# Optimization experiments

Measured on AMD Instinct MI355X. Metric: run time of the kernel, lower is better.

## Reference

```python
import jax, jax.numpy as jnp
import numpy as np

N_G, K = 1024, 64
n_G, k = 32, 8          # n_G = sqrt(N_G), k = sqrt(K)
m = n_G * k             # 256
M = N_G * K             # 65536

def _mask_indices(k):
    # concentric square rings of a k x k grid; ring 0 = outermost
    ii, jj = np.meshgrid(np.arange(k), np.arange(k), indexing='ij')
    d = np.minimum(np.minimum(ii, jj), np.minimum(k - 1 - ii, k - 1 - jj))
    rings = [(d == r) for r in range((k + 1) // 2)]
    groups = np.array_split(np.arange(len(rings)), 3)  # outer / inter / inner ring groups
    merged = [np.any(np.stack([rings[i] for i in g]), axis=0) for g in groups]
    outer, inter, inner = merged
    flat = lambda msk: np.nonzero(msk.ravel())[0]
    return flat(inner), flat(inter), flat(outer)

IDX_INNER, IDX_INTER, IDX_OUTER = _mask_indices(k)  # sizes 4, 12, 48

def setup_inputs() -> dict:
    key = jax.random.key(0)
    ks = jax.random.split(key, 13)
    p = lambda kk, sh: 0.05 * jax.random.normal(kk, sh, dtype=jnp.float32)
    return {
        'pgi': jax.random.normal(ks[0], (32, M, 3), dtype=jnp.float32),
        'W_lift': p(ks[1], (3, 32)),   'b_lift': p(ks[2], (32,)),
        'W_code': p(ks[3], (96, 128)), 'b_code': p(ks[4], (128,)),
        'W_h1': p(ks[5], (128, 64)),   'b_h1': p(ks[6], (64,)),
        'W_h2': p(ks[7], (64, 32)),    'b_h2': p(ks[8], (32,)),
        'W_h3': p(ks[9], (32, 16)),    'b_h3': p(ks[10], (16,)),
        'W_h4': p(ks[11], (16, 3)),    'b_h4': jnp.zeros((3,), jnp.float32),
    }

def _lift_max(pts, W, b):
    # pts: [B, N_G, n_sel, 3] -> SMLP(3->32, leakyrelu 0.2) -> max over points
    h = jax.nn.leaky_relu(jnp.einsum('bgpc,cd->bgpd', pts, W) + b, 0.2)
    return h.max(axis=2)  # [B, N_G, 32]

def reference(pgi, W_lift, b_lift, W_code, b_code, W_h1, b_h1, W_h2, b_h2, W_h3, b_h3, W_h4, b_h4):
    B = pgi.shape[0]
    # pgi [B, M, 3] is a row-major m x m grid; partition into N_G blocks of k x k points
    grid = pgi.reshape(B, n_G, k, n_G, k, 3)
    blocks = grid.transpose(0, 1, 3, 2, 4, 5).reshape(B, N_G, K, 3)
    v_inner = _lift_max(blocks[:, :, IDX_INNER], W_lift, b_lift)
    v_inter = _lift_max(blocks[:, :, IDX_INTER], W_lift, b_lift)
    v_outer = _lift_max(blocks[:, :, IDX_OUTER], W_lift, b_lift)
    v = jnp.concatenate([v_inner, v_inter, v_outer], axis=-1)   # [B, N_G, 96]
    v_code = jax.nn.leaky_relu(v @ W_code + b_code, 0.2)        # [B, N_G, 128]
    h = jax.nn.relu(v_code @ W_h1 + b_h1)
    h = jax.nn.relu(h @ W_h2 + b_h2)
    h = jax.nn.relu(h @ W_h3 + b_h3)
    return h @ W_h4 + b_h4                                      # guidance_pts [B, N_G, 3]
```

## Files before the change

### kernel.cpp

```cpp
#include <hip/hip_runtime.h>
#include <math.h>

constexpr int SV  = 100;
constexpr int SC  = 132;
constexpr int SH1 = 68;
constexpr int SH2 = 36;
constexpr int SH3 = 20;

__global__ __launch_bounds__(256, 2)
void flatnet_fused(const float* __restrict__ pgi,
                   const float* __restrict__ Wl, const float* __restrict__ bl,
                   const float* __restrict__ Wc, const float* __restrict__ bc,
                   const float* __restrict__ W1, const float* __restrict__ b1,
                   const float* __restrict__ W2, const float* __restrict__ b2,
                   const float* __restrict__ W3, const float* __restrict__ b3,
                   const float* __restrict__ W4, const float* __restrict__ b4,
                   float* __restrict__ out)
{
    __shared__ float sA[64 * SV];
    __shared__ float sB[64 * SC];

    const int t   = threadIdx.x;
    const int blk = blockIdx.x;

    {
        const int ln = t >> 2;
        const int q  = t & 3;
        const int gn = blk * 64 + ln;
        const int b  = gn >> 10;
        const int g  = gn & 1023;
        const int gi = g >> 5, gj = g & 31;

        float w0[8], w1[8], w2[8], bb[8];
        #pragma unroll
        for (int d = 0; d < 8; ++d) {
            const int dd = q * 8 + d;
            w0[d] = Wl[dd];
            w1[d] = Wl[32 + dd];
            w2[d] = Wl[64 + dd];
            bb[d] = bl[dd];
        }

        float gm[3][8];
        #pragma unroll
        for (int gg = 0; gg < 3; ++gg)
            #pragma unroll
            for (int d = 0; d < 8; ++d) gm[gg][d] = -INFINITY;

        constexpr int GT[8][8] = {
            {2,2,2,2,2,2,2,2},
            {2,2,2,2,2,2,2,2},
            {2,2,1,1,1,1,2,2},
            {2,2,1,0,0,1,2,2},
            {2,2,1,0,0,1,2,2},
            {2,2,1,1,1,1,2,2},
            {2,2,2,2,2,2,2,2},
            {2,2,2,2,2,2,2,2},
        };

        const size_t rowbase = (size_t)b * 65536 + ((size_t)gi * 8) * 256 + (size_t)gj * 8;
        #pragma unroll
        for (int pi = 0; pi < 8; ++pi) {
            const float4* src = (const float4*)(pgi + (rowbase + (size_t)pi * 256) * 3);
            float f[24];
            #pragma unroll
            for (int l = 0; l < 6; ++l) {
                const float4 v = src[l];
                f[l*4+0] = v.x; f[l*4+1] = v.y; f[l*4+2] = v.z; f[l*4+3] = v.w;
            }
            #pragma unroll
            for (int pj = 0; pj < 8; ++pj) {
                const int grp = GT[pi][pj];
                const float x = f[pj*3], y = f[pj*3+1], z = f[pj*3+2];
                #pragma unroll
                for (int d = 0; d < 8; ++d) {
                    float v = fmaf(x, w0[d], bb[d]);
                    v = fmaf(y, w1[d], v);
                    v = fmaf(z, w2[d], v);
                    v = fmaxf(v, 0.2f * v);
                    gm[grp][d] = fmaxf(gm[grp][d], v);
                }
            }
        }
        #pragma unroll
        for (int gg = 0; gg < 3; ++gg) {
            float4 lo = make_float4(gm[gg][0], gm[gg][1], gm[gg][2], gm[gg][3]);
            float4 hi = make_float4(gm[gg][4], gm[gg][5], gm[gg][6], gm[gg][7]);
            *(float4*)&sA[ln*SV + gg*32 + q*8]     = lo;
            *(float4*)&sA[ln*SV + gg*32 + q*8 + 4] = hi;
        }
    }
    __syncthreads();

    {
        const int ri = t >> 5;
        const int c0 = (t & 31) * 4;
        float acc[8][4];
        {
            const float4 bv = *(const float4*)&bc[c0];
            #pragma unroll
            for (int r = 0; r < 8; ++r) { acc[r][0]=bv.x; acc[r][1]=bv.y; acc[r][2]=bv.z; acc[r][3]=bv.w; }
        }
        for (int j = 0; j < 96; j += 4) {
            float4 a[8];
            #pragma unroll
            for (int r = 0; r < 8; ++r) a[r] = *(const float4*)&sA[(ri*8+r)*SV + j];
            #pragma unroll
            for (int jj = 0; jj < 4; ++jj) {
                const float4 w = *(const float4*)&Wc[(j+jj)*128 + c0];
                #pragma unroll
                for (int r = 0; r < 8; ++r) {
                    const float av = (jj==0)?a[r].x:(jj==1)?a[r].y:(jj==2)?a[r].z:a[r].w;
                    acc[r][0] = fmaf(av, w.x, acc[r][0]);
                    acc[r][1] = fmaf(av, w.y, acc[r][1]);
                    acc[r][2] = fmaf(av, w.z, acc[r][2]);
                    acc[r][3] = fmaf(av, w.w, acc[r][3]);
                }
            }
        }
        #pragma unroll
        for (int r = 0; r < 8; ++r) {
            float4 o;
            o.x = fmaxf(acc[r][0], 0.2f*acc[r][0]);
            o.y = fmaxf(acc[r][1], 0.2f*acc[r][1]);
            o.z = fmaxf(acc[r][2], 0.2f*acc[r][2]);
            o.w = fmaxf(acc[r][3], 0.2f*acc[r][3]);
            *(float4*)&sB[(ri*8+r)*SC + c0] = o;
        }
    }
    __syncthreads();

    {
        const int ri = t >> 4;
        const int c0 = (t & 15) * 4;
        float acc[4][4];
        {
            const float4 bv = *(const float4*)&b1[c0];
            #pragma unroll
            for (int r = 0; r < 4; ++r) { acc[r][0]=bv.x; acc[r][1]=bv.y; acc[r][2]=bv.z; acc[r][3]=bv.w; }
        }
        for (int j = 0; j < 128; j += 4) {
            float4 a[4];
            #pragma unroll
            for (int r = 0; r < 4; ++r) a[r] = *(const float4*)&sB[(ri*4+r)*SC + j];
            #pragma unroll
            for (int jj = 0; jj < 4; ++jj) {
                const float4 w = *(const float4*)&W1[(j+jj)*64 + c0];
                #pragma unroll
                for (int r = 0; r < 4; ++r) {
                    const float av = (jj==0)?a[r].x:(jj==1)?a[r].y:(jj==2)?a[r].z:a[r].w;
                    acc[r][0] = fmaf(av, w.x, acc[r][0]);
                    acc[r][1] = fmaf(av, w.y, acc[r][1]);
                    acc[r][2] = fmaf(av, w.z, acc[r][2]);
                    acc[r][3] = fmaf(av, w.w, acc[r][3]);
                }
            }
        }
        #pragma unroll
        for (int r = 0; r < 4; ++r) {
            float4 o;
            o.x = fmaxf(acc[r][0], 0.f); o.y = fmaxf(acc[r][1], 0.f);
            o.z = fmaxf(acc[r][2], 0.f); o.w = fmaxf(acc[r][3], 0.f);
            *(float4*)&sA[(ri*4+r)*SH1 + c0] = o;
        }
    }
    __syncthreads();

    {
        const int ri = t >> 3;
        const int c0 = (t & 7) * 4;
        float acc[2][4];
        {
            const float4 bv = *(const float4*)&b2[c0];
            #pragma unroll
            for (int r = 0; r < 2; ++r) { acc[r][0]=bv.x; acc[r][1]=bv.y; acc[r][2]=bv.z; acc[r][3]=bv.w; }
        }
        for (int j = 0; j < 64; j += 4) {
            float4 a[2];
            #pragma unroll
            for (int r = 0; r < 2; ++r) a[r] = *(const float4*)&sA[(ri*2+r)*SH1 + j];
            #pragma unroll
            for (int jj = 0; jj < 4; ++jj) {
                const float4 w = *(const float4*)&W2[(j+jj)*32 + c0];
                #pragma unroll
                for (int r = 0; r < 2; ++r) {
                    const float av = (jj==0)?a[r].x:(jj==1)?a[r].y:(jj==2)?a[r].z:a[r].w;
                    acc[r][0] = fmaf(av, w.x, acc[r][0]);
                    acc[r][1] = fmaf(av, w.y, acc[r][1]);
                    acc[r][2] = fmaf(av, w.z, acc[r][2]);
                    acc[r][3] = fmaf(av, w.w, acc[r][3]);
                }
            }
        }
        #pragma unroll
        for (int r = 0; r < 2; ++r) {
            float4 o;
            o.x = fmaxf(acc[r][0], 0.f); o.y = fmaxf(acc[r][1], 0.f);
            o.z = fmaxf(acc[r][2], 0.f); o.w = fmaxf(acc[r][3], 0.f);
            *(float4*)&sB[(ri*2+r)*SH2 + c0] = o;
        }
    }
    __syncthreads();

    {
        const int row = t >> 2;
        const int c0  = (t & 3) * 4;
        float acc[4];
        {
            const float4 bv = *(const float4*)&b3[c0];
            acc[0]=bv.x; acc[1]=bv.y; acc[2]=bv.z; acc[3]=bv.w;
        }
        for (int j = 0; j < 32; j += 4) {
            const float4 a = *(const float4*)&sB[row*SH2 + j];
            #pragma unroll
            for (int jj = 0; jj < 4; ++jj) {
                const float4 w = *(const float4*)&W3[(j+jj)*16 + c0];
                const float av = (jj==0)?a.x:(jj==1)?a.y:(jj==2)?a.z:a.w;
                acc[0] = fmaf(av, w.x, acc[0]);
                acc[1] = fmaf(av, w.y, acc[1]);
                acc[2] = fmaf(av, w.z, acc[2]);
                acc[3] = fmaf(av, w.w, acc[3]);
            }
        }
        float4 o;
        o.x = fmaxf(acc[0], 0.f); o.y = fmaxf(acc[1], 0.f);
        o.z = fmaxf(acc[2], 0.f); o.w = fmaxf(acc[3], 0.f);
        *(float4*)&sA[row*SH3 + c0] = o;
    }
    __syncthreads();

    if (t < 64) {
        float acc0 = b4[0], acc1 = b4[1], acc2 = b4[2];
        float a[16];
        #pragma unroll
        for (int l = 0; l < 4; ++l) {
            const float4 v = *(const float4*)&sA[t*SH3 + l*4];
            a[l*4+0]=v.x; a[l*4+1]=v.y; a[l*4+2]=v.z; a[l*4+3]=v.w;
        }
        #pragma unroll
        for (int j = 0; j < 16; ++j) {
            acc0 = fmaf(a[j], W4[j*3+0], acc0);
            acc1 = fmaf(a[j], W4[j*3+1], acc1);
            acc2 = fmaf(a[j], W4[j*3+2], acc2);
        }
        const size_t gn = (size_t)blk * 64 + t;
        out[gn*3 + 0] = acc0;
        out[gn*3 + 1] = acc1;
        out[gn*3 + 2] = acc2;
    }
}

extern "C" void kernel_launch(void* const* d_in, const int* in_sizes, int n_in,
                              void* d_out, int out_size, void* d_ws, size_t ws_size,
                              hipStream_t stream)
{
    const float* pgi = (const float*)d_in[0];
    const float* Wl  = (const float*)d_in[1];
    const float* bl  = (const float*)d_in[2];
    const float* Wc  = (const float*)d_in[3];
    const float* bc  = (const float*)d_in[4];
    const float* W1  = (const float*)d_in[5];
    const float* b1  = (const float*)d_in[6];
    const float* W2  = (const float*)d_in[7];
    const float* b2  = (const float*)d_in[8];
    const float* W3  = (const float*)d_in[9];
    const float* b3  = (const float*)d_in[10];
    const float* W4  = (const float*)d_in[11];
    const float* b4  = (const float*)d_in[12];

    hipLaunchKernelGGL(flatnet_fused, dim3(512), dim3(256), 0, stream,
                       pgi, Wl, bl, Wc, bc, W1, b1, W2, b2, W3, b3, W4, b4,
                       (float*)d_out);
}
```

Baseline: 118.0 us.

## Halve groups per block, split block rows across thread pairs, defer leaky-relu

Each block now handles 32 point groups instead of 64, which doubles the grid to 1024 blocks and raises launch bounds to 4 blocks per CU. In the lift stage, each group's 8 rows are split between two threads, each taking four mirrored rows so one shared ring table covers both halves. The partial maxima are merged with a cross-lane shuffle. Leaky-relu is monotonic, so it moves after the max and runs once per channel instead of once per point. The MLP stages are retiled for 32 rows, which means more blocks and better latency hiding but a lower register budget and less weight reuse per block.

Result: slower. 128.1 us (+8.5%).

```diff
diff --git a/kernel.cpp b/kernel.cpp
--- a/kernel.cpp
+++ b/kernel.cpp
@@ -7,7 +7,7 @@
 constexpr int SH2 = 36;
 constexpr int SH3 = 20;
 
-__global__ __launch_bounds__(256, 2)
+__global__ __launch_bounds__(256, 4)
 void flatnet_fused(const float* __restrict__ pgi,
                    const float* __restrict__ Wl, const float* __restrict__ bl,
                    const float* __restrict__ Wc, const float* __restrict__ bc,
@@ -17,16 +17,18 @@
                    const float* __restrict__ W4, const float* __restrict__ b4,
                    float* __restrict__ out)
 {
-    __shared__ float sA[64 * SV];
-    __shared__ float sB[64 * SC];
+    __shared__ float sA[32 * SV];
+    __shared__ float sB[32 * SC];
 
     const int t   = threadIdx.x;
     const int blk = blockIdx.x;
 
     {
-        const int ln = t >> 2;
-        const int q  = t & 3;
-        const int gn = blk * 64 + ln;
+        const int ln = t >> 3;
+        const int q  = t & 7;
+        const int dq = (q & 3) * 8;
+        const int h  = q >> 2;
+        const int gn = blk * 32 + ln;
         const int b  = gn >> 10;
         const int g  = gn & 1023;
         const int gi = g >> 5, gj = g & 31;
@@ -34,11 +36,10 @@
         float w0[8], w1[8], w2[8], bb[8];
         #pragma unroll
         for (int d = 0; d < 8; ++d) {
-            const int dd = q * 8 + d;
-            w0[d] = Wl[dd];
-            w1[d] = Wl[32 + dd];
-            w2[d] = Wl[64 + dd];
-            bb[d] = bl[dd];
+            w0[d] = Wl[dq + d];
+            w1[d] = Wl[32 + dq + d];
+            w2[d] = Wl[64 + dq + d];
+            bb[d] = bl[dq + d];
         }
 
         float gm[3][8];
@@ -47,21 +48,18 @@
             #pragma unroll
             for (int d = 0; d < 8; ++d) gm[gg][d] = -INFINITY;
 
-        constexpr int GT[8][8] = {
+        constexpr int GT4[4][8] = {
             {2,2,2,2,2,2,2,2},
             {2,2,2,2,2,2,2,2},
             {2,2,1,1,1,1,2,2},
             {2,2,1,0,0,1,2,2},
-            {2,2,1,0,0,1,2,2},
-            {2,2,1,1,1,1,2,2},
-            {2,2,2,2,2,2,2,2},
-            {2,2,2,2,2,2,2,2},
         };
 
         const size_t rowbase = (size_t)b * 65536 + ((size_t)gi * 8) * 256 + (size_t)gj * 8;
         #pragma unroll
-        for (int pi = 0; pi < 8; ++pi) {
-            const float4* src = (const float4*)(pgi + (rowbase + (size_t)pi * 256) * 3);
+        for (int pi = 0; pi < 4; ++pi) {
+            const int prow = h ? (7 - pi) : pi;
+            const float4* src = (const float4*)(pgi + (rowbase + (size_t)prow * 256) * 3);
             float f[24];
             #pragma unroll
             for (int l = 0; l < 6; ++l) {
@@ -70,24 +68,38 @@
             }
             #pragma unroll
             for (int pj = 0; pj < 8; ++pj) {
-                const int grp = GT[pi][pj];
+                const int grp = GT4[pi][pj];
                 const float x = f[pj*3], y = f[pj*3+1], z = f[pj*3+2];
                 #pragma unroll
                 for (int d = 0; d < 8; ++d) {
                     float v = fmaf(x, w0[d], bb[d]);
                     v = fmaf(y, w1[d], v);
                     v = fmaf(z, w2[d], v);
-                    v = fmaxf(v, 0.2f * v);
                     gm[grp][d] = fmaxf(gm[grp][d], v);
                 }
             }
         }
         #pragma unroll
-        for (int gg = 0; gg < 3; ++gg) {
-            float4 lo = make_float4(gm[gg][0], gm[gg][1], gm[gg][2], gm[gg][3]);
-            float4 hi = make_float4(gm[gg][4], gm[gg][5], gm[gg][6], gm[gg][7]);
-            *(float4*)&sA[ln*SV + gg*32 + q*8]     = lo;
-            *(float4*)&sA[ln*SV + gg*32 + q*8 + 4] = hi;
+        for (int gg = 0; gg < 3; ++gg)
+            #pragma unroll
+            for (int d = 0; d < 8; ++d)
+                gm[gg][d] = fmaxf(gm[gg][d], __shfl_xor(gm[gg][d], 4));
+
+        if (h == 0) {
+            #pragma unroll
+            for (int gg = 0; gg < 3; ++gg) {
+                float4 lo, hi;
+                lo.x = fmaxf(gm[gg][0], 0.2f*gm[gg][0]);
+                lo.y = fmaxf(gm[gg][1], 0.2f*gm[gg][1]);
+                lo.z = fmaxf(gm[gg][2], 0.2f*gm[gg][2]);
+                lo.w = fmaxf(gm[gg][3], 0.2f*gm[gg][3]);
+                hi.x = fmaxf(gm[gg][4], 0.2f*gm[gg][4]);
+                hi.y = fmaxf(gm[gg][5], 0.2f*gm[gg][5]);
+                hi.z = fmaxf(gm[gg][6], 0.2f*gm[gg][6]);
+                hi.w = fmaxf(gm[gg][7], 0.2f*gm[gg][7]);
+                *(float4*)&sA[ln*SV + gg*32 + dq]     = lo;
+                *(float4*)&sA[ln*SV + gg*32 + dq + 4] = hi;
+            }
         }
     }
     __syncthreads();
@@ -95,57 +107,19 @@
     {
         const int ri = t >> 5;
         const int c0 = (t & 31) * 4;
-        float acc[8][4];
+        float acc[4][4];
         {
             const float4 bv = *(const float4*)&bc[c0];
             #pragma unroll
-            for (int r = 0; r < 8; ++r) { acc[r][0]=bv.x; acc[r][1]=bv.y; acc[r][2]=bv.z; acc[r][3]=bv.w; }
+            for (int r = 0; r < 4; ++r) { acc[r][0]=bv.x; acc[r][1]=bv.y; acc[r][2]=bv.z; acc[r][3]=bv.w; }
         }
         for (int j = 0; j < 96; j += 4) {
-            float4 a[8];
-            #pragma unroll
-            for (int r = 0; r < 8; ++r) a[r] = *(const float4*)&sA[(ri*8+r)*SV + j];
+            float4 a[4];
+            #pragma unroll
+            for (int r = 0; r < 4; ++r) a[r] = *(const float4*)&sA[(ri*4+r)*SV + j];
             #pragma unroll
             for (int jj = 0; jj < 4; ++jj) {
                 const float4 w = *(const float4*)&Wc[(j+jj)*128 + c0];
-                #pragma unroll
-                for (int r = 0; r < 8; ++r) {
-                    const float av = (jj==0)?a[r].x:(jj==1)?a[r].y:(jj==2)?a[r].z:a[r].w;
-                    acc[r][0] = fmaf(av, w.x, acc[r][0]);
-                    acc[r][1] = fmaf(av, w.y, acc[r][1]);
-                    acc[r][2] = fmaf(av, w.z, acc[r][2]);
-                    acc[r][3] = fmaf(av, w.w, acc[r][3]);
-                }
-            }
-        }
-        #pragma unroll
-        for (int r = 0; r < 8; ++r) {
-            float4 o;
-            o.x = fmaxf(acc[r][0], 0.2f*acc[r][0]);
-            o.y = fmaxf(acc[r][1], 0.2f*acc[r][1]);
-            o.z = fmaxf(acc[r][2], 0.2f*acc[r][2]);
-            o.w = fmaxf(acc[r][3], 0.2f*acc[r][3]);
-            *(float4*)&sB[(ri*8+r)*SC + c0] = o;
-        }
-    }
-    __syncthreads();
-
-    {
-        const int ri = t >> 4;
-        const int c0 = (t & 15) * 4;
-        float acc[4][4];
-        {
-            const float4 bv = *(const float4*)&b1[c0];
-            #pragma unroll
-            for (int r = 0; r < 4; ++r) { acc[r][0]=bv.x; acc[r][1]=bv.y; acc[r][2]=bv.z; acc[r][3]=bv.w; }
-        }
-        for (int j = 0; j < 128; j += 4) {
-            float4 a[4];
-            #pragma unroll
-            for (int r = 0; r < 4; ++r) a[r] = *(const float4*)&sB[(ri*4+r)*SC + j];
-            #pragma unroll
-            for (int jj = 0; jj < 4; ++jj) {
-                const float4 w = *(const float4*)&W1[(j+jj)*64 + c0];
                 #pragma unroll
                 for (int r = 0; r < 4; ++r) {
                     const float av = (jj==0)?a[r].x:(jj==1)?a[r].y:(jj==2)?a[r].z:a[r].w;
@@ -159,29 +133,31 @@
         #pragma unroll
         for (int r = 0; r < 4; ++r) {
             float4 o;
-            o.x = fmaxf(acc[r][0], 0.f); o.y = fmaxf(acc[r][1], 0.f);
-            o.z = fmaxf(acc[r][2], 0.f); o.w = fmaxf(acc[r][3], 0.f);
-            *(float4*)&sA[(ri*4+r)*SH1 + c0] = o;
-        }
-    }
-    __syncthreads();
-
-    {
-        const int ri = t >> 3;
-        const int c0 = (t & 7) * 4;
+            o.x = fmaxf(acc[r][0], 0.2f*acc[r][0]);
+            o.y = fmaxf(acc[r][1], 0.2f*acc[r][1]);
+            o.z = fmaxf(acc[r][2], 0.2f*acc[r][2]);
+            o.w = fmaxf(acc[r][3], 0.2f*acc[r][3]);
+            *(float4*)&sB[(ri*4+r)*SC + c0] = o;
+        }
+    }
+    __syncthreads();
+
+    {
+        const int ri = t >> 4;
+        const int c0 = (t & 15) * 4;
         float acc[2][4];
         {
-            const float4 bv = *(const float4*)&b2[c0];
+            const float4 bv = *(const float4*)&b1[c0];
             #pragma unroll
             for (int r = 0; r < 2; ++r) { acc[r][0]=bv.x; acc[r][1]=bv.y; acc[r][2]=bv.z; acc[r][3]=bv.w; }
         }
-        for (int j = 0; j < 64; j += 4) {
+        for (int j = 0; j < 128; j += 4) {
             float4 a[2];
             #pragma unroll
-            for (int r = 0; r < 2; ++r) a[r] = *(const float4*)&sA[(ri*2+r)*SH1 + j];
-            #pragma unroll
-            for (int jj = 0; jj < 4; ++jj) {
-                const float4 w = *(const float4*)&W2[(j+jj)*32 + c0];
+            for (int r = 0; r < 2; ++r) a[r] = *(const float4*)&sB[(ri*2+r)*SC + j];
+            #pragma unroll
+            for (int jj = 0; jj < 4; ++jj) {
+                const float4 w = *(const float4*)&W1[(j+jj)*64 + c0];
                 #pragma unroll
                 for (int r = 0; r < 2; ++r) {
                     const float av = (jj==0)?a[r].x:(jj==1)?a[r].y:(jj==2)?a[r].z:a[r].w;
@@ -197,12 +173,39 @@
             float4 o;
             o.x = fmaxf(acc[r][0], 0.f); o.y = fmaxf(acc[r][1], 0.f);
             o.z = fmaxf(acc[r][2], 0.f); o.w = fmaxf(acc[r][3], 0.f);
-            *(float4*)&sB[(ri*2+r)*SH2 + c0] = o;
-        }
-    }
-    __syncthreads();
-
-    {
+            *(float4*)&sA[(ri*2+r)*SH1 + c0] = o;
+        }
+    }
+    __syncthreads();
+
+    {
+        const int row = t >> 3;
+        const int c0  = (t & 7) * 4;
+        float acc[4];
+        {
+            const float4 bv = *(const float4*)&b2[c0];
+            acc[0]=bv.x; acc[1]=bv.y; acc[2]=bv.z; acc[3]=bv.w;
+        }
+        for (int j = 0; j < 64; j += 4) {
+            const float4 a = *(const float4*)&sA[row*SH1 + j];
+            #pragma unroll
+            for (int jj = 0; jj < 4; ++jj) {
+                const float4 w = *(const float4*)&W2[(j+jj)*32 + c0];
+                const float av = (jj==0)?a.x:(jj==1)?a.y:(jj==2)?a.z:a.w;
+                acc[0] = fmaf(av, w.x, acc[0]);
+                acc[1] = fmaf(av, w.y, acc[1]);
+                acc[2] = fmaf(av, w.z, acc[2]);
+                acc[3] = fmaf(av, w.w, acc[3]);
+            }
+        }
+        float4 o;
+        o.x = fmaxf(acc[0], 0.f); o.y = fmaxf(acc[1], 0.f);
+        o.z = fmaxf(acc[2], 0.f); o.w = fmaxf(acc[3], 0.f);
+        *(float4*)&sB[row*SH2 + c0] = o;
+    }
+    __syncthreads();
+
+    if (t < 128) {
         const int row = t >> 2;
         const int c0  = (t & 3) * 4;
         float acc[4];
@@ -229,7 +232,7 @@
     }
     __syncthreads();
 
-    if (t < 64) {
+    if (t < 32) {
         float acc0 = b4[0], acc1 = b4[1], acc2 = b4[2];
         float a[16];
         #pragma unroll
@@ -243,7 +246,7 @@
             acc1 = fmaf(a[j], W4[j*3+1], acc1);
             acc2 = fmaf(a[j], W4[j*3+2], acc2);
         }
-        const size_t gn = (size_t)blk * 64 + t;
+        const size_t gn = (size_t)blk * 32 + t;
         out[gn*3 + 0] = acc0;
         out[gn*3 + 1] = acc1;
         out[gn*3 + 2] = acc2;
@@ -268,7 +271,7 @@
     const float* W4  = (const float*)d_in[11];
     const float* b4  = (const float*)d_in[12];
 
-    hipLaunchKernelGGL(flatnet_fused, dim3(512), dim3(256), 0, stream,
+    hipLaunchKernelGGL(flatnet_fused, dim3(1024), dim3(256), 0, stream,
                        pgi, Wl, bl, Wc, bc, W1, b1, W2, b2, W3, b3, W4, b4,
                        (float*)d_out);
 }
```

## Transpose activation tiles and split output columns per wavefront for uniform weight loads

Applied to the files above, without the earlier changes.

Activations in shared memory are now stored feature-major with a padded stride of 65, so each lane owns one point and reads a single conflict-free word per input feature. Each wavefront computes a contiguous slice of output columns, which makes weight addresses wave-uniform so they can be fetched with scalar loads. The leaky-relu in the lift stage is moved after the max reduction, which is valid because the activation is monotonic, and this removes per-point work. The trade-offs are larger per-thread accumulator arrays, more shared-memory footprint, and the final layer now using only three wavefronts.

New measurement: 128.4 us. +8.8%, slower.

```diff
diff --git a/kernel.cpp b/kernel.cpp
--- a/kernel.cpp
+++ b/kernel.cpp
@@ -1,11 +1,7 @@
 #include <hip/hip_runtime.h>
 #include <math.h>
 
-constexpr int SV  = 100;
-constexpr int SC  = 132;
-constexpr int SH1 = 68;
-constexpr int SH2 = 36;
-constexpr int SH3 = 20;
+constexpr int ST = 65;
 
 __global__ __launch_bounds__(256, 2)
 void flatnet_fused(const float* __restrict__ pgi,
@@ -17,11 +13,13 @@
                    const float* __restrict__ W4, const float* __restrict__ b4,
                    float* __restrict__ out)
 {
-    __shared__ float sA[64 * SV];
-    __shared__ float sB[64 * SC];
+    __shared__ float sA[96  * ST];
+    __shared__ float sB[128 * ST];
 
-    const int t   = threadIdx.x;
-    const int blk = blockIdx.x;
+    const int t    = threadIdx.x;
+    const int blk  = blockIdx.x;
+    const int lane = t & 63;
+    const int wv   = __builtin_amdgcn_readfirstlane(t >> 6);
 
     {
         const int ln = t >> 2;
@@ -77,176 +75,100 @@
                     float v = fmaf(x, w0[d], bb[d]);
                     v = fmaf(y, w1[d], v);
                     v = fmaf(z, w2[d], v);
-                    v = fmaxf(v, 0.2f * v);
                     gm[grp][d] = fmaxf(gm[grp][d], v);
                 }
             }
         }
         #pragma unroll
-        for (int gg = 0; gg < 3; ++gg) {
-            float4 lo = make_float4(gm[gg][0], gm[gg][1], gm[gg][2], gm[gg][3]);
-            float4 hi = make_float4(gm[gg][4], gm[gg][5], gm[gg][6], gm[gg][7]);
-            *(float4*)&sA[ln*SV + gg*32 + q*8]     = lo;
-            *(float4*)&sA[ln*SV + gg*32 + q*8 + 4] = hi;
+        for (int gg = 0; gg < 3; ++gg)
+            #pragma unroll
+            for (int d = 0; d < 8; ++d) {
+                const float v = gm[gg][d];
+                sA[(gg*32 + q*8 + d) * ST + ln] = fmaxf(v, 0.2f * v);
+            }
+    }
+    __syncthreads();
+
+    {
+        const float* wp = Wc + (wv << 5);
+        const float* bp = bc + (wv << 5);
+        float acc[32];
+        #pragma unroll
+        for (int c = 0; c < 32; ++c) acc[c] = bp[c];
+        for (int j = 0; j < 96; ++j) {
+            const float a = sA[j * ST + lane];
+            #pragma unroll
+            for (int c = 0; c < 32; ++c)
+                acc[c] = fmaf(a, wp[j*128 + c], acc[c]);
+        }
+        #pragma unroll
+        for (int c = 0; c < 32; ++c) {
+            const float v = acc[c];
+            sB[((wv << 5) + c) * ST + lane] = fmaxf(v, 0.2f * v);
         }
     }
     __syncthreads();
 
     {
-        const int ri = t >> 5;
-        const int c0 = (t & 31) * 4;
-        float acc[8][4];
-        {
-            const float4 bv = *(const float4*)&bc[c0];
+        const float* wp = W1 + (wv << 4);
+        const float* bp = b1 + (wv << 4);
+        float acc[16];
+        #pragma unroll
+        for (int c = 0; c < 16; ++c) acc[c] = bp[c];
+        for (int j = 0; j < 128; ++j) {
+            const float a = sB[j * ST + lane];
             #pragma unroll
-            for (int r = 0; r < 8; ++r) { acc[r][0]=bv.x; acc[r][1]=bv.y; acc[r][2]=bv.z; acc[r][3]=bv.w; }
-        }
-        for (int j = 0; j < 96; j += 4) {
-            float4 a[8];
-            #pragma unroll
-            for (int r = 0; r < 8; ++r) a[r] = *(const float4*)&sA[(ri*8+r)*SV + j];
-            #pragma unroll
-            for (int jj = 0; jj < 4; ++jj) {
-                const float4 w = *(const float4*)&Wc[(j+jj)*128 + c0];
-                #pragma unroll
-                for (int r = 0; r < 8; ++r) {
-                    const float av = (jj==0)?a[r].x:(jj==1)?a[r].y:(jj==2)?a[r].z:a[r].w;
-                    acc[r][0] = fmaf(av, w.x, acc[r][0]);
-                    acc[r][1] = fmaf(av, w.y, acc[r][1]);
-                    acc[r][2] = fmaf(av, w.z, acc[r][2]);
-                    acc[r][3] = fmaf(av, w.w, acc[r][3]);
-                }
-            }
+            for (int c = 0; c < 16; ++c)
+                acc[c] = fmaf(a, wp[j*64 + c], acc[c]);
         }
         #pragma unroll
-        for (int r = 0; r < 8; ++r) {
-            float4 o;
-            o.x = fmaxf(acc[r][0], 0.2f*acc[r][0]);
-            o.y = fmaxf(acc[r][1], 0.2f*acc[r][1]);
-            o.z = fmaxf(acc[r][2], 0.2f*acc[r][2]);
-            o.w = fmaxf(acc[r][3], 0.2f*acc[r][3]);
-            *(float4*)&sB[(ri*8+r)*SC + c0] = o;
-        }
+        for (int c = 0; c < 16; ++c)
+            sA[((wv << 4) + c) * ST + lane] = fmaxf(acc[c], 0.f);
     }
     __syncthreads();
 
     {
-        const int ri = t >> 4;
-        const int c0 = (t & 15) * 4;
-        float acc[4][4];
-        {
-            const float4 bv = *(const float4*)&b1[c0];
+        const float* wp = W2 + (wv << 3);
+        const float* bp = b2 + (wv << 3);
+        float acc[8];
+        #pragma unroll
+        for (int c = 0; c < 8; ++c) acc[c] = bp[c];
+        for (int j = 0; j < 64; ++j) {
+            const float a = sA[j * ST + lane];
             #pragma unroll
-            for (int r = 0; r < 4; ++r) { acc[r][0]=bv.x; acc[r][1]=bv.y; acc[r][2]=bv.z; acc[r][3]=bv.w; }
-        }
-        for (int j = 0; j < 128; j += 4) {
-            float4 a[4];
-            #pragma unroll
-            for (int r = 0; r < 4; ++r) a[r] = *(const float4*)&sB[(ri*4+r)*SC + j];
-            #pragma unroll
-            for (int jj = 0; jj < 4; ++jj) {
-                const float4 w = *(const float4*)&W1[(j+jj)*64 + c0];
-                #pragma unroll
-                for (int r = 0; r < 4; ++r) {
-                    const float av = (jj==0)?a[r].x:(jj==1)?a[r].y:(jj==2)?a[r].z:a[r].w;
-                    acc[r][0] = fmaf(av, w.x, acc[r][0]);
-                    acc[r][1] = fmaf(av, w.y, acc[r][1]);
-                    acc[r][2] = fmaf(av, w.z, acc[r][2]);
-                    acc[r][3] = fmaf(av, w.w, acc[r][3]);
-                }
-            }
+            for (int c = 0; c < 8; ++c)
+                acc[c] = fmaf(a, wp[j*32 + c], acc[c]);
         }
         #pragma unroll
-        for (int r = 0; r < 4; ++r) {
-            float4 o;
-            o.x = fmaxf(acc[r][0], 0.f); o.y = fmaxf(acc[r][1], 0.f);
-            o.z = fmaxf(acc[r][2], 0.f); o.w = fmaxf(acc[r][3], 0.f);
-            *(float4*)&sA[(ri*4+r)*SH1 + c0] = o;
-        }
+        for (int c = 0; c < 8; ++c)
+            sB[((wv << 3) + c) * ST + lane] = fmaxf(acc[c], 0.f);
     }
     __syncthreads();
 
     {
-        const int ri = t >> 3;
-        const int c0 = (t & 7) * 4;
-        float acc[2][4];
-        {
-            const float4 bv = *(const float4*)&b2[c0];
+        const float* wp = W3 + (wv << 2);
+        const float* bp = b3 + (wv << 2);
+        float acc[4];
+        #pragma unroll
+        for (int c = 0; c < 4; ++c) acc[c] = bp[c];
+        for (int j = 0; j < 32; ++j) {
+            const float a = sB[j * ST + lane];
             #pragma unroll
-            for (int r = 0; r < 2; ++r) { acc[r][0]=bv.x; acc[r][1]=bv.y; acc[r][2]=bv.z; acc[r][3]=bv.w; }
-        }
-        for (int j = 0; j < 64; j += 4) {
-            float4 a[2];
-            #pragma unroll
-            for (int r = 0; r < 2; ++r) a[r] = *(const float4*)&sA[(ri*2+r)*SH1 + j];
-            #pragma unroll
-            for (int jj = 0; jj < 4; ++jj) {
-                const float4 w = *(const float4*)&W2[(j+jj)*32 + c0];
-                #pragma unroll
-                for (int r = 0; r < 2; ++r) {
-                    const float av = (jj==0)?a[r].x:(jj==1)?a[r].y:(jj==2)?a[r].z:a[r].w;
-                    acc[r][0] = fmaf(av, w.x, acc[r][0]);
-                    acc[r][1] = fmaf(av, w.y, acc[r][1]);
-                    acc[r][2] = fmaf(av, w.z, acc[r][2]);
-                    acc[r][3] = fmaf(av, w.w, acc[r][3]);
-                }
-            }
+            for (int c = 0; c < 4; ++c)
+                acc[c] = fmaf(a, wp[j*16 + c], acc[c]);
         }
         #pragma unroll
-        for (int r = 0; r < 2; ++r) {
-            float4 o;
-            o.x = fmaxf(acc[r][0], 0.f); o.y = fmaxf(acc[r][1], 0.f);
-            o.z = fmaxf(acc[r][2], 0.f); o.w = fmaxf(acc[r][3], 0.f);
-            *(float4*)&sB[(ri*2+r)*SH2 + c0] = o;
-        }
+        for (int c = 0; c < 4; ++c)
+            sA[((wv << 2) + c) * ST + lane] = fmaxf(acc[c], 0.f);
     }
     __syncthreads();
 
-    {
-        const int row = t >> 2;
-        const int c0  = (t & 3) * 4;
-        float acc[4];
-        {
-            const float4 bv = *(const float4*)&b3[c0];
-            acc[0]=bv.x; acc[1]=bv.y; acc[2]=bv.z; acc[3]=bv.w;
-        }
-        for (int j = 0; j < 32; j += 4) {
-            const float4 a = *(const float4*)&sB[row*SH2 + j];
-            #pragma unroll
-            for (int jj = 0; jj < 4; ++jj) {
-                const float4 w = *(const float4*)&W3[(j+jj)*16 + c0];
-                const float av = (jj==0)?a.x:(jj==1)?a.y:(jj==2)?a.z:a.w;
-                acc[0] = fmaf(av, w.x, acc[0]);
-                acc[1] = fmaf(av, w.y, acc[1]);
-                acc[2] = fmaf(av, w.z, acc[2]);
-                acc[3] = fmaf(av, w.w, acc[3]);
-            }
-        }
-        float4 o;
-        o.x = fmaxf(acc[0], 0.f); o.y = fmaxf(acc[1], 0.f);
-        o.z = fmaxf(acc[2], 0.f); o.w = fmaxf(acc[3], 0.f);
-        *(float4*)&sA[row*SH3 + c0] = o;
-    }
-    __syncthreads();
-
-    if (t < 64) {
-        float acc0 = b4[0], acc1 = b4[1], acc2 = b4[2];
-        float a[16];
+    if (wv < 3) {
+        float acc = b4[wv];
         #pragma unroll
-        for (int l = 0; l < 4; ++l) {
-            const float4 v = *(const float4*)&sA[t*SH3 + l*4];
-            a[l*4+0]=v.x; a[l*4+1]=v.y; a[l*4+2]=v.z; a[l*4+3]=v.w;
-        }
-        #pragma unroll
-        for (int j = 0; j < 16; ++j) {
-            acc0 = fmaf(a[j], W4[j*3+0], acc0);
-            acc1 = fmaf(a[j], W4[j*3+1], acc1);
-            acc2 = fmaf(a[j], W4[j*3+2], acc2);
-        }
-        const size_t gn = (size_t)blk * 64 + t;
-        out[gn*3 + 0] = acc0;
-        out[gn*3 + 1] = acc1;
-        out[gn*3 + 2] = acc2;
+        for (int j = 0; j < 16; ++j)
+            acc = fmaf(sA[j * ST + lane], W4[j*3 + wv], acc);
+        out[((size_t)blk * 64 + lane) * 3 + wv] = acc;
     }
 }
 
```

## Hoist leaky-relu past max, retile MLP GEMMs with register prefetch

Applied to the files above, without the earlier changes.

Moves the leaky-ReLU from every lifted point to after the max-pool, which is valid because leaky-ReLU is monotonic, and removes per-point multiply/max work. The code and h1 GEMMs are retiled to 4x8 and 2x8 per-thread output tiles so each weight float4 is reused across more columns. Weight and activation tiles are prefetched into registers one k-step ahead, and the first weights are loaded before the barrier. This raises register pressure under launch_bounds(256,2).

After: 125.9 us. 6.7% more time.

```diff
diff --git a/kernel.cpp b/kernel.cpp
--- a/kernel.cpp
+++ b/kernel.cpp
@@ -77,155 +77,235 @@
                     float v = fmaf(x, w0[d], bb[d]);
                     v = fmaf(y, w1[d], v);
                     v = fmaf(z, w2[d], v);
-                    v = fmaxf(v, 0.2f * v);
                     gm[grp][d] = fmaxf(gm[grp][d], v);
                 }
             }
         }
         #pragma unroll
         for (int gg = 0; gg < 3; ++gg) {
-            float4 lo = make_float4(gm[gg][0], gm[gg][1], gm[gg][2], gm[gg][3]);
-            float4 hi = make_float4(gm[gg][4], gm[gg][5], gm[gg][6], gm[gg][7]);
+            float4 lo, hi;
+            lo.x = fmaxf(gm[gg][0], 0.2f*gm[gg][0]);
+            lo.y = fmaxf(gm[gg][1], 0.2f*gm[gg][1]);
+            lo.z = fmaxf(gm[gg][2], 0.2f*gm[gg][2]);
+            lo.w = fmaxf(gm[gg][3], 0.2f*gm[gg][3]);
+            hi.x = fmaxf(gm[gg][4], 0.2f*gm[gg][4]);
+            hi.y = fmaxf(gm[gg][5], 0.2f*gm[gg][5]);
+            hi.z = fmaxf(gm[gg][6], 0.2f*gm[gg][6]);
+            hi.w = fmaxf(gm[gg][7], 0.2f*gm[gg][7]);
             *(float4*)&sA[ln*SV + gg*32 + q*8]     = lo;
             *(float4*)&sA[ln*SV + gg*32 + q*8 + 4] = hi;
         }
     }
-    __syncthreads();
-
-    {
-        const int ri = t >> 5;
-        const int c0 = (t & 31) * 4;
-        float acc[8][4];
+
+    const int p1r0 = (t >> 4) << 2;
+    const int p1c0 = (t & 15) << 3;
+
+    float4 w0c[4], w1c[4];
+    #pragma unroll
+    for (int jj = 0; jj < 4; ++jj) {
+        w0c[jj] = *(const float4*)&Wc[jj*128 + p1c0];
+        w1c[jj] = *(const float4*)&Wc[jj*128 + p1c0 + 4];
+    }
+    float acc1[4][8];
+    {
+        const float4 bv0 = *(const float4*)&bc[p1c0];
+        const float4 bv1 = *(const float4*)&bc[p1c0 + 4];
+        #pragma unroll
+        for (int r = 0; r < 4; ++r) {
+            acc1[r][0]=bv0.x; acc1[r][1]=bv0.y; acc1[r][2]=bv0.z; acc1[r][3]=bv0.w;
+            acc1[r][4]=bv1.x; acc1[r][5]=bv1.y; acc1[r][6]=bv1.z; acc1[r][7]=bv1.w;
+        }
+    }
+    __syncthreads();
+
+    {
+        float4 a_c[4];
+        #pragma unroll
+        for (int r = 0; r < 4; ++r) a_c[r] = *(const float4*)&sA[(p1r0+r)*SV];
+
+        for (int j = 0; j < 96; j += 4) {
+            const int jn = (j + 4 < 96) ? (j + 4) : 0;
+            float4 a_n[4], w0n[4], w1n[4];
+            #pragma unroll
+            for (int jj = 0; jj < 4; ++jj) {
+                w0n[jj] = *(const float4*)&Wc[(jn+jj)*128 + p1c0];
+                w1n[jj] = *(const float4*)&Wc[(jn+jj)*128 + p1c0 + 4];
+            }
+            #pragma unroll
+            for (int r = 0; r < 4; ++r) a_n[r] = *(const float4*)&sA[(p1r0+r)*SV + jn];
+
+            #pragma unroll
+            for (int jj = 0; jj < 4; ++jj) {
+                const float4 wl = w0c[jj], wh = w1c[jj];
+                const float wv[8] = {wl.x,wl.y,wl.z,wl.w,wh.x,wh.y,wh.z,wh.w};
+                #pragma unroll
+                for (int r = 0; r < 4; ++r) {
+                    const float av = (jj==0)?a_c[r].x:(jj==1)?a_c[r].y:(jj==2)?a_c[r].z:a_c[r].w;
+                    #pragma unroll
+                    for (int c = 0; c < 8; ++c)
+                        acc1[r][c] = fmaf(av, wv[c], acc1[r][c]);
+                }
+            }
+            #pragma unroll
+            for (int r = 0; r < 4; ++r) a_c[r] = a_n[r];
+            #pragma unroll
+            for (int jj = 0; jj < 4; ++jj) { w0c[jj] = w0n[jj]; w1c[jj] = w1n[jj]; }
+        }
+        #pragma unroll
+        for (int r = 0; r < 4; ++r) {
+            float4 lo, hi;
+            lo.x = fmaxf(acc1[r][0], 0.2f*acc1[r][0]);
+            lo.y = fmaxf(acc1[r][1], 0.2f*acc1[r][1]);
+            lo.z = fmaxf(acc1[r][2], 0.2f*acc1[r][2]);
+            lo.w = fmaxf(acc1[r][3], 0.2f*acc1[r][3]);
+            hi.x = fmaxf(acc1[r][4], 0.2f*acc1[r][4]);
+            hi.y = fmaxf(acc1[r][5], 0.2f*acc1[r][5]);
+            hi.z = fmaxf(acc1[r][6], 0.2f*acc1[r][6]);
+            hi.w = fmaxf(acc1[r][7], 0.2f*acc1[r][7]);
+            *(float4*)&sB[(p1r0+r)*SC + p1c0]     = lo;
+            *(float4*)&sB[(p1r0+r)*SC + p1c0 + 4] = hi;
+        }
+    }
+    __syncthreads();
+
+    {
+        const int r0 = (t >> 3) << 1;
+        const int c0 = (t & 7) << 3;
+        float acc[2][8];
         {
-            const float4 bv = *(const float4*)&bc[c0];
-            #pragma unroll
-            for (int r = 0; r < 8; ++r) { acc[r][0]=bv.x; acc[r][1]=bv.y; acc[r][2]=bv.z; acc[r][3]=bv.w; }
-        }
-        for (int j = 0; j < 96; j += 4) {
-            float4 a[8];
-            #pragma unroll
-            for (int r = 0; r < 8; ++r) a[r] = *(const float4*)&sA[(ri*8+r)*SV + j];
-            #pragma unroll
-            for (int jj = 0; jj < 4; ++jj) {
-                const float4 w = *(const float4*)&Wc[(j+jj)*128 + c0];
+            const float4 bv0 = *(const float4*)&b1[c0];
+            const float4 bv1 = *(const float4*)&b1[c0 + 4];
+            #pragma unroll
+            for (int r = 0; r < 2; ++r) {
+                acc[r][0]=bv0.x; acc[r][1]=bv0.y; acc[r][2]=bv0.z; acc[r][3]=bv0.w;
+                acc[r][4]=bv1.x; acc[r][5]=bv1.y; acc[r][6]=bv1.z; acc[r][7]=bv1.w;
+            }
+        }
+        float4 w0c2[4], w1c2[4], a_c[2];
+        #pragma unroll
+        for (int jj = 0; jj < 4; ++jj) {
+            w0c2[jj] = *(const float4*)&W1[jj*64 + c0];
+            w1c2[jj] = *(const float4*)&W1[jj*64 + c0 + 4];
+        }
+        #pragma unroll
+        for (int r = 0; r < 2; ++r) a_c[r] = *(const float4*)&sB[(r0+r)*SC];
+
+        for (int j = 0; j < 128; j += 4) {
+            const int jn = (j + 4 < 128) ? (j + 4) : 0;
+            float4 a_n[2], w0n[4], w1n[4];
+            #pragma unroll
+            for (int jj = 0; jj < 4; ++jj) {
+                w0n[jj] = *(const float4*)&W1[(jn+jj)*64 + c0];
+                w1n[jj] = *(const float4*)&W1[(jn+jj)*64 + c0 + 4];
+            }
+            #pragma unroll
+            for (int r = 0; r < 2; ++r) a_n[r] = *(const float4*)&sB[(r0+r)*SC + jn];
+
+            #pragma unroll
+            for (int jj = 0; jj < 4; ++jj) {
+                const float4 wl = w0c2[jj], wh = w1c2[jj];
+                const float wv[8] = {wl.x,wl.y,wl.z,wl.w,wh.x,wh.y,wh.z,wh.w};
                 #pragma unroll
-                for (int r = 0; r < 8; ++r) {
-                    const float av = (jj==0)?a[r].x:(jj==1)?a[r].y:(jj==2)?a[r].z:a[r].w;
+                for (int r = 0; r < 2; ++r) {
+                    const float av = (jj==0)?a_c[r].x:(jj==1)?a_c[r].y:(jj==2)?a_c[r].z:a_c[r].w;
+                    #pragma unroll
+                    for (int c = 0; c < 8; ++c)
+                        acc[r][c] = fmaf(av, wv[c], acc[r][c]);
+                }
+            }
+            #pragma unroll
+            for (int r = 0; r < 2; ++r) a_c[r] = a_n[r];
+            #pragma unroll
+            for (int jj = 0; jj < 4; ++jj) { w0c2[jj] = w0n[jj]; w1c2[jj] = w1n[jj]; }
+        }
+        #pragma unroll
+        for (int r = 0; r < 2; ++r) {
+            float4 lo, hi;
+            lo.x = fmaxf(acc[r][0], 0.f); lo.y = fmaxf(acc[r][1], 0.f);
+            lo.z = fmaxf(acc[r][2], 0.f); lo.w = fmaxf(acc[r][3], 0.f);
+            hi.x = fmaxf(acc[r][4], 0.f); hi.y = fmaxf(acc[r][5], 0.f);
+            hi.z = fmaxf(acc[r][6], 0.f); hi.w = fmaxf(acc[r][7], 0.f);
+            *(float4*)&sA[(r0+r)*SH1 + c0]     = lo;
+            *(float4*)&sA[(r0+r)*SH1 + c0 + 4] = hi;
+        }
+    }
+    __syncthreads();
+
+    {
+        const int r0 = (t >> 3) << 1;
+        const int c0 = (t & 7) << 2;
+        float acc[2][4];
+        {
+            const float4 bv = *(const float4*)&b2[c0];
+            #pragma unroll
+            for (int r = 0; r < 2; ++r) { acc[r][0]=bv.x; acc[r][1]=bv.y; acc[r][2]=bv.z; acc[r][3]=bv.w; }
+        }
+        float4 wc3[4], a_c[2];
+        #pragma unroll
+        for (int jj = 0; jj < 4; ++jj) wc3[jj] = *(const float4*)&W2[jj*32 + c0];
+        #pragma unroll
+        for (int r = 0; r < 2; ++r) a_c[r] = *(const float4*)&sA[(r0+r)*SH1];
+
+        for (int j = 0; j < 64; j += 4) {
+            const int jn = (j + 4 < 64) ? (j + 4) : 0;
+            float4 a_n[2], wn[4];
+            #pragma unroll
+            for (int jj = 0; jj < 4; ++jj) wn[jj] = *(const float4*)&W2[(jn+jj)*32 + c0];
+            #pragma unroll
+            for (int r = 0; r < 2; ++r) a_n[r] = *(const float4*)&sA[(r0+r)*SH1 + jn];
+
+            #pragma unroll
+            for (int jj = 0; jj < 4; ++jj) {
+                const float4 w = wc3[jj];
+                #pragma unroll
+                for (int r = 0; r < 2; ++r) {
+                    const float av = (jj==0)?a_c[r].x:(jj==1)?a_c[r].y:(jj==2)?a_c[r].z:a_c[r].w;
                     acc[r][0] = fmaf(av, w.x, acc[r][0]);
                     acc[r][1] = fmaf(av, w.y, acc[r][1]);
                     acc[r][2] = fmaf(av, w.z, acc[r][2]);
                     acc[r][3] = fmaf(av, w.w, acc[r][3]);
                 }
             }
-        }
-        #pragma unroll
-        for (int r = 0; r < 8; ++r) {
-            float4 o;
-            o.x = fmaxf(acc[r][0], 0.2f*acc[r][0]);
-            o.y = fmaxf(acc[r][1], 0.2f*acc[r][1]);
-            o.z = fmaxf(acc[r][2], 0.2f*acc[r][2]);
-            o.w = fmaxf(acc[r][3], 0.2f*acc[r][3]);
-            *(float4*)&sB[(ri*8+r)*SC + c0] = o;
-        }
-    }
-    __syncthreads();
-
-    {
-        const int ri = t >> 4;
-        const int c0 = (t & 15) * 4;
-        float acc[4][4];
-        {
-            const float4 bv = *(const float4*)&b1[c0];
-            #pragma unroll
-            for (int r = 0; r < 4; ++r) { acc[r][0]=bv.x; acc[r][1]=bv.y; acc[r][2]=bv.z; acc[r][3]=bv.w; }
-        }
-        for (int j = 0; j < 128; j += 4) {
-            float4 a[4];
-            #pragma unroll
-            for (int r = 0; r < 4; ++r) a[r] = *(const float4*)&sB[(ri*4+r)*SC + j];
-            #pragma unroll
-            for (int jj = 0; jj < 4; ++jj) {
-                const float4 w = *(const float4*)&W1[(j+jj)*64 + c0];
-                #pragma unroll
-                for (int r = 0; r < 4; ++r) {
-                    const float av = (jj==0)?a[r].x:(jj==1)?a[r].y:(jj==2)?a[r].z:a[r].w;
-                    acc[r][0] = fmaf(av, w.x, acc[r][0]);
-                    acc[r][1] = fmaf(av, w.y, acc[r][1]);
-                    acc[r][2] = fmaf(av, w.z, acc[r][2]);
-                    acc[r][3] = fmaf(av, w.w, acc[r][3]);
-                }
-            }
-        }
-        #pragma unroll
-        for (int r = 0; r < 4; ++r) {
-            float4 o;
-            o.x = fmaxf(acc[r][0], 0.f); o.y = fmaxf(acc[r][1], 0.f);
-            o.z = fmaxf(acc[r][2], 0.f); o.w = fmaxf(acc[r][3], 0.f);
-            *(float4*)&sA[(ri*4+r)*SH1 + c0] = o;
-        }
-    }
-    __syncthreads();
-
-    {
-        const int ri = t >> 3;
-        const int c0 = (t & 7) * 4;
-        float acc[2][4];
-        {
-            const float4 bv = *(const float4*)&b2[c0];
-            #pragma unroll
-            for (int r = 0; r < 2; ++r) { acc[r][0]=bv.x; acc[r][1]=bv.y; acc[r][2]=bv.z; acc[r][3]=bv.w; }
-        }
-        for (int j = 0; j < 64; j += 4) {
-            float4 a[2];
-            #pragma unroll
-            for (int r = 0; r < 2; ++r) a[r] = *(const float4*)&sA[(ri*2+r)*SH1 + j];
-            #pragma unroll
-            for (int jj = 0; jj < 4; ++jj) {
-                const float4 w = *(const float4*)&W2[(j+jj)*32 + c0];
-                #pragma unroll
-                for (int r = 0; r < 2; ++r) {
-                    const float av = (jj==0)?a[r].x:(jj==1)?a[r].y:(jj==2)?a[r].z:a[r].w;
-                    acc[r][0] = fmaf(av, w.x, acc[r][0]);
-                    acc[r][1] = fmaf(av, w.y, acc[r][1]);
-                    acc[r][2] = fmaf(av, w.z, acc[r][2]);
-                    acc[r][3] = fmaf(av, w.w, acc[r][3]);
-                }
-            }
+            #pragma unroll
+            for (int r = 0; r < 2; ++r) a_c[r] = a_n[r];
+            #pragma unroll
+            for (int jj = 0; jj < 4; ++jj) wc3[jj] = wn[jj];
         }
         #pragma unroll
         for (int r = 0; r < 2; ++r) {
             float4 o;
             o.x = fmaxf(acc[r][0], 0.f); o.y = fmaxf(acc[r][1], 0.f);
             o.z = fmaxf(acc[r][2], 0.f); o.w = fmaxf(acc[r][3], 0.f);
-            *(float4*)&sB[(ri*2+r)*SH2 + c0] = o;
-        }
-    }
-    __syncthreads();
-
-    {
-        const int row = t >> 2;
-        const int c0  = (t & 3) * 4;
+            *(float4*)&sB[(r0+r)*SH2 + c0] = o;
+        }
+    }
+    __syncthreads();
+
+    {
+        const int r  = t >> 2;
+        const int c0 = (t & 3) << 2;
         float acc[4];
         {
             const float4 bv = *(const float4*)&b3[c0];
             acc[0]=bv.x; acc[1]=bv.y; acc[2]=bv.z; acc[3]=bv.w;
         }
+        #pragma unroll
         for (int j = 0; j < 32; j += 4) {
-            const float4 a = *(const float4*)&sB[row*SH2 + j];
+            const float4 A = *(const float4*)&sB[r*SH2 + j];
+            const float af[4] = {A.x, A.y, A.z, A.w};
             #pragma unroll
             for (int jj = 0; jj < 4; ++jj) {
                 const float4 w = *(const float4*)&W3[(j+jj)*16 + c0];
-                const float av = (jj==0)?a.x:(jj==1)?a.y:(jj==2)?a.z:a.w;
-                acc[0] = fmaf(av, w.x, acc[0]);
-                acc[1] = fmaf(av, w.y, acc[1]);
-                acc[2] = fmaf(av, w.z, acc[2]);
-                acc[3] = fmaf(av, w.w, acc[3]);
+                acc[0] = fmaf(af[jj], w.x, acc[0]);
+                acc[1] = fmaf(af[jj], w.y, acc[1]);
+                acc[2] = fmaf(af[jj], w.z, acc[2]);
+                acc[3] = fmaf(af[jj], w.w, acc[3]);
             }
         }
         float4 o;
         o.x = fmaxf(acc[0], 0.f); o.y = fmaxf(acc[1], 0.f);
         o.z = fmaxf(acc[2], 0.f); o.w = fmaxf(acc[3], 0.f);
-        *(float4*)&sA[row*SH3 + c0] = o;
+        *(float4*)&sA[r*SH3 + c0] = o;
     }
     __syncthreads();
 
```
